# Kernel tuning notes

Hardware: AMD Instinct MI355X
Metric: run time of the kernel (lower is better)

## Reference

```python
import jax, jax.numpy as jnp
import numpy as np

E = 256  # embed_dim (hardcoded in source module)
H = 4    # n_head
D = E // H
SEQ = 32768


def setup_inputs() -> dict:
    key = jax.random.key(0)
    ks = jax.random.split(key, 5)
    x = jax.random.normal(ks[0], (SEQ, E), dtype=jnp.float32)
    in_proj_weight = jax.random.normal(ks[1], (3 * E, E), dtype=jnp.float32) * (1.0 / np.sqrt(E))
    in_proj_bias = jax.random.normal(ks[2], (3 * E,), dtype=jnp.float32) * 0.02
    out_proj_weight = jax.random.normal(ks[3], (E, E), dtype=jnp.float32) * (1.0 / np.sqrt(E))
    out_proj_bias = jax.random.normal(ks[4], (E,), dtype=jnp.float32) * 0.02
    return {
        "x": x,
        "in_proj_weight": in_proj_weight,
        "in_proj_bias": in_proj_bias,
        "out_proj_weight": out_proj_weight,
        "out_proj_bias": out_proj_bias,
    }


def reference(x, in_proj_weight, in_proj_bias, out_proj_weight, out_proj_bias):
    # QKV projections (q uses only the first token of x: single-query decode attention)
    Wq, Wk, Wv = in_proj_weight[:E], in_proj_weight[E:2 * E], in_proj_weight[2 * E:]
    bq, bk, bv = in_proj_bias[:E], in_proj_bias[E:2 * E], in_proj_bias[2 * E:]
    q = x[:1] @ Wq.T + bq            # [1, E]
    k = x @ Wk.T + bk                # [S, E]
    v = x @ Wv.T + bv                # [S, E]

    qh = q.reshape(H, D)             # [H, D] (single query)
    kh = k.reshape(-1, H, D)         # [S, H, D]
    vh = v.reshape(-1, H, D)         # [S, H, D]

    scale = 1.0 / np.sqrt(D).astype(np.float32)
    scores = jnp.einsum("hd,shd->hs", qh, kh) * scale   # [H, S]
    attn = jax.nn.softmax(scores, axis=-1)                # [H, S]
    ctx = jnp.einsum("hs,shd->hd", attn, vh)             # [H, D]

    out = ctx.reshape(1, E) @ out_proj_weight.T + out_proj_bias  # [1, E]
    return out
```

## Files before the change

kernel.cpp:

```cpp
#include <hip/hip_runtime.h>
#include <hip/hip_cooperative_groups.h>
namespace cg = cooperative_groups;

#define NBLK 256
#define WS_LP   0
#define WS_YV   1024
#define WS_B2   2048
#define WS_KQ   2304
#define WS_C4   3328
#define WS_M2   3392
#define WS_YP   265536

__device__ __forceinline__ float dot4(float4 a, float4 b) {
  return a.x * b.x + a.y * b.y + a.z * b.z + a.w * b.w;
}

__device__ __forceinline__ void phaseA_dist(const float* __restrict__ x, const float* __restrict__ W,
                                            const float* __restrict__ inb, float* __restrict__ kq,
                                            float* __restrict__ c4, float* qls, int bid, int t) {
  const int lane = t & 63, w = t >> 6;
  const int h = bid >> 6;
  const int c0 = (bid & 63) * 4;
  const int rloc = lane >> 3, sub = lane & 7;
  const int row = h * 64 + w * 8 + rloc;
  const float4* w4 = (const float4*)&W[(size_t)row * 256 + sub * 32];
  const float4* x4 = (const float4*)&x[sub * 32];
  float p = 0.f;
#pragma unroll
  for (int j = 0; j < 8; ++j) p += dot4(w4[j], x4[j]);
  p += __shfl_xor(p, 1);
  p += __shfl_xor(p, 2);
  p += __shfl_xor(p, 4);
  if (sub == 0) qls[w * 8 + rloc] = p + inb[row];
  __syncthreads();
  if (w < 4) {
    float v = W[(size_t)(256 + h * 64 + lane) * 256 + (c0 + w)] * qls[lane];
#pragma unroll
    for (int m = 1; m < 64; m <<= 1) v += __shfl_xor(v, m);
    if (lane == 0) kq[h * 256 + c0 + w] = v;
  } else if (w == 4 && (bid & 63) == 0) {
    float v = inb[256 + h * 64 + lane] * qls[lane];
#pragma unroll
    for (int m = 1; m < 64; m <<= 1) v += __shfl_xor(v, m);
    if (lane == 0) c4[h] = v;
  }
}

__device__ __forceinline__ void phaseA_m2(const float* __restrict__ W, const float* __restrict__ Wout,
                                          float* __restrict__ M2, float* sh, int b2, int t) {
  float* wout_t = sh;
  const int tile = b2 >> 1, sub = b2 & 1;
  const int h = tile >> 4, e0 = (tile & 15) * 16 + sub * 8;
  {
    const int e = t >> 6, d = t & 63;
    wout_t[e * 64 + d] = Wout[(size_t)(e0 + e) * 256 + h * 64 + d];
  }
  __syncthreads();
  const int c = t & 255, eh = t >> 8;
  float acc[4] = {0.f, 0.f, 0.f, 0.f};
#pragma unroll 8
  for (int d = 0; d < 64; ++d) {
    const float wv = W[(size_t)(512 + h * 64 + d) * 256 + c];
#pragma unroll
    for (int e = 0; e < 4; ++e) acc[e] += wv * wout_t[(eh * 4 + e) * 64 + d];
  }
#pragma unroll
  for (int e = 0; e < 4; ++e)
    M2[(size_t)(e0 + eh * 4 + e) * 1024 + h * 256 + c] = acc[e];
}

__device__ __forceinline__ void phaseA_b2(const float* __restrict__ Wout, const float* __restrict__ inb,
                                          const float* __restrict__ bout, float* __restrict__ bias2,
                                          float* sh, int b, int t) {
  float* red = sh;
  const int og = t >> 5, seg = t & 31;
  const int e = b * 16 + og;
  float acc = 0.f;
#pragma unroll
  for (int j = 0; j < 8; ++j)
    acc += Wout[(size_t)e * 256 + seg * 8 + j] * inb[512 + seg * 8 + j];
  red[og * 32 + seg] = acc;
  __syncthreads();
  if (t < 16) {
    float s = bout[b * 16 + t];
#pragma unroll
    for (int i = 0; i < 32; ++i) s += red[t * 32 + i];
    bias2[b * 16 + t] = s;
  }
}

__device__ __forceinline__ float bscore(float4 xv, float4 kq0, float4 kq1, float4 kq2,
                                        float4 kq3, float c4v, int lane) {
  float p0 = dot4(xv, kq0), p1 = dot4(xv, kq1), p2 = dot4(xv, kq2), p3 = dot4(xv, kq3);
  const bool b1 = (lane & 2) != 0;
  float keep0 = b1 ? p2 : p0, send0 = b1 ? p0 : p2;
  keep0 += __shfl_xor(send0, 2);
  float keep1 = b1 ? p3 : p1, send1 = b1 ? p1 : p3;
  keep1 += __shfl_xor(send1, 2);
  const bool b0 = (lane & 1) != 0;
  float vv = b0 ? keep1 : keep0, sv = b0 ? keep0 : keep1;
  vv += __shfl_xor(sv, 1);
  vv += __shfl_xor(vv, 4);
  vv += __shfl_xor(vv, 8);
  vv += __shfl_xor(vv, 16);
  vv += __shfl_xor(vv, 32);
  return (vv + c4v) * 0.125f;
}

__device__ __forceinline__ void phaseB_core(const float4* xvA, const float4* xvB,
                                            const float* __restrict__ kq, const float* __restrict__ c4,
                                            float* __restrict__ ypart, float* __restrict__ lpart,
                                            float* yls, int bid, int t) {
  float* sll = yls + 8192;
  const int lane = t & 63, w = t >> 6;
  const int hme = lane & 3;
  const float4 kq0 = *(const float4*)&kq[0 * 256 + lane * 4];
  const float4 kq1 = *(const float4*)&kq[1 * 256 + lane * 4];
  const float4 kq2 = *(const float4*)&kq[2 * 256 + lane * 4];
  const float4 kq3 = *(const float4*)&kq[3 * 256 + lane * 4];
  const float c4v = c4[hme];

  float vA[8], vB[8];
#pragma unroll
  for (int r = 0; r < 8; ++r) vA[r] = bscore(xvA[r], kq0, kq1, kq2, kq3, c4v, lane);
#pragma unroll
  for (int r = 0; r < 8; ++r) vB[r] = bscore(xvB[r], kq0, kq1, kq2, kq3, c4v, lane);

  float l = 0.f;
  float4 a[4];
#pragma unroll
  for (int k = 0; k < 4; ++k) a[k] = (float4){0.f, 0.f, 0.f, 0.f};
#pragma unroll
  for (int r = 0; r < 8; ++r) {
    const float e0 = __expf(vA[r]);
    l += e0;
    const float e1 = __shfl_xor(e0, 1);
    const float e2 = __shfl_xor(e0, 2);
    const float e3 = __shfl_xor(e0, 3);
    a[0].x += e0 * xvA[r].x; a[0].y += e0 * xvA[r].y; a[0].z += e0 * xvA[r].z; a[0].w += e0 * xvA[r].w;
    a[1].x += e1 * xvA[r].x; a[1].y += e1 * xvA[r].y; a[1].z += e1 * xvA[r].z; a[1].w += e1 * xvA[r].w;
    a[2].x += e2 * xvA[r].x; a[2].y += e2 * xvA[r].y; a[2].z += e2 * xvA[r].z; a[2].w += e2 * xvA[r].w;
    a[3].x += e3 * xvA[r].x; a[3].y += e3 * xvA[r].y; a[3].z += e3 * xvA[r].z; a[3].w += e3 * xvA[r].w;
  }
#pragma unroll
  for (int r = 0; r < 8; ++r) {
    const float e0 = __expf(vB[r]);
    l += e0;
    const float e1 = __shfl_xor(e0, 1);
    const float e2 = __shfl_xor(e0, 2);
    const float e3 = __shfl_xor(e0, 3);
    a[0].x += e0 * xvB[r].x; a[0].y += e0 * xvB[r].y; a[0].z += e0 * xvB[r].z; a[0].w += e0 * xvB[r].w;
    a[1].x += e1 * xvB[r].x; a[1].y += e1 * xvB[r].y; a[1].z += e1 * xvB[r].z; a[1].w += e1 * xvB[r].w;
    a[2].x += e2 * xvB[r].x; a[2].y += e2 * xvB[r].y; a[2].z += e2 * xvB[r].z; a[2].w += e2 * xvB[r].w;
    a[3].x += e3 * xvB[r].x; a[3].y += e3 * xvB[r].y; a[3].z += e3 * xvB[r].z; a[3].w += e3 * xvB[r].w;
  }

  __syncthreads();
  if (lane < 4) sll[w * 4 + lane] = l;
#pragma unroll
  for (int k = 0; k < 4; ++k) {
    const int h = hme ^ k;
    *(float4*)&yls[w * 1024 + h * 256 + lane * 4] = a[k];
  }
  __syncthreads();

  if (t < 4) {
    float lb = 0.f;
#pragma unroll
    for (int i = 0; i < 8; ++i) lb += sll[i * 4 + t];
    lpart[t * NBLK + bid] = lb;
  }
  float* yp = &ypart[(size_t)bid * 1024];
#pragma unroll
  for (int o = t; o < 1024; o += 512) {
    float s = 0.f;
#pragma unroll
    for (int i = 0; i < 8; ++i) s += yls[i * 1024 + o];
    yp[o] = s;
  }
}

__device__ __forceinline__ void phaseC(const float* __restrict__ ypart, const float* __restrict__ lpart,
                                       float* __restrict__ z, float* sh, int bid, int t) {
  float* lred = sh;
  float* sred = sh + 256;
  const int h = bid >> 4;
  const int o0 = bid * 16;
  if (t < 256) lred[t] = lpart[h * 256 + t];
  __syncthreads();
  for (int s = 128; s > 0; s >>= 1) {
    if (t < s) lred[t] += lred[t + s];
    __syncthreads();
  }
  const float inv = 1.0f / lred[0];
  const int ol = t & 15, bg = t >> 4;
  float s = 0.f;
#pragma unroll
  for (int j = 0; j < 8; ++j) {
    const int b = bg * 8 + j;
    s += ypart[(size_t)b * 1024 + o0 + ol];
  }
  sred[bg * 16 + ol] = s;
  __syncthreads();
  if (t < 16) {
    float tot = 0.f;
#pragma unroll
    for (int g = 0; g < 32; ++g) tot += sred[g * 16 + t];
    z[o0 + t] = tot * inv;
  }
}

__device__ __forceinline__ void phaseD(const float* __restrict__ M2, const float* __restrict__ z,
                                       const float* __restrict__ bias2, float* __restrict__ out,
                                       float* sh, int bid, int t) {
  float* zls = sh;
  float* smo = sh + 1024;
  for (int i = t; i < 1024; i += 512) zls[i] = z[i];
  __syncthreads();
  const int og = t >> 5, seg = t & 31;
  const int e = bid * 16 + og;
  float acc = 0.f;
  const float4* m4 = (const float4*)&M2[(size_t)e * 1024 + seg * 32];
  const float4* z4 = (const float4*)&zls[seg * 32];
#pragma unroll
  for (int j = 0; j < 8; ++j) acc += dot4(m4[j], z4[j]);
  smo[og * 32 + seg] = acc;
  __syncthreads();
  if (t < 16) {
    float s = bias2[bid * 16 + t];
#pragma unroll
    for (int i = 0; i < 32; ++i) s += smo[t * 32 + i];
    out[bid * 16 + t] = s;
  }
}

__global__ void __launch_bounds__(512, 1) mha_coop(const float* __restrict__ x,
                                                   const float* __restrict__ W,
                                                   const float* __restrict__ inb,
                                                   const float* __restrict__ Wout,
                                                   const float* __restrict__ bout,
                                                   float* __restrict__ out,
                                                   float* __restrict__ ws) {
  __shared__ __align__(16) float sh[8224];
  const int t = threadIdx.x, bid = blockIdx.x;
  const int lane = t & 63, w = t >> 6;
  cg::grid_group grid = cg::this_grid();

  const int r0 = bid * 128 + w * 16;
  float4 xvA[8], xvB[8];
#pragma unroll
  for (int r = 0; r < 8; ++r)
    xvA[r] = *(const float4*)&x[(size_t)(r0 + r) * 256 + lane * 4];
#pragma unroll
  for (int r = 0; r < 8; ++r)
    xvB[r] = *(const float4*)&x[(size_t)(r0 + 8 + r) * 256 + lane * 4];

  phaseA_dist(x, W, inb, ws + WS_KQ, ws + WS_C4, sh, bid, t);

  grid.sync();
  phaseB_core(xvA, xvB, ws + WS_KQ, ws + WS_C4, ws + WS_YP, ws + WS_LP, sh, bid, t);
  grid.sync();
  if (bid < 64) phaseC(ws + WS_YP, ws + WS_LP, ws + WS_YV, sh, bid, t);
  else if (bid < 192) phaseA_m2(W, Wout, ws + WS_M2, sh, bid - 64, t);
  else if (bid < 208) phaseA_b2(Wout, inb, bout, ws + WS_B2, sh, bid - 192, t);
  grid.sync();
  if (bid < 16) phaseD(ws + WS_M2, ws + WS_YV, ws + WS_B2, out, sh, bid, t);
}

__global__ void __launch_bounds__(512) fb_A(const float* __restrict__ x, const float* __restrict__ W,
                                            const float* __restrict__ inb, float* __restrict__ ws) {
  __shared__ __align__(16) float sh[64];
  phaseA_dist(x, W, inb, ws + WS_KQ, ws + WS_C4, sh, blockIdx.x, threadIdx.x);
}
__global__ void __launch_bounds__(512) fb_B(const float* __restrict__ x, float* __restrict__ ws) {
  __shared__ __align__(16) float sh[8224];
  const int bid = blockIdx.x, t = threadIdx.x;
  const int lane = t & 63, w = t >> 6;
  const int r0 = bid * 128 + w * 16;
  float4 xvA[8], xvB[8];
#pragma unroll
  for (int r = 0; r < 8; ++r)
    xvA[r] = *(const float4*)&x[(size_t)(r0 + r) * 256 + lane * 4];
#pragma unroll
  for (int r = 0; r < 8; ++r)
    xvB[r] = *(const float4*)&x[(size_t)(r0 + 8 + r) * 256 + lane * 4];
  phaseB_core(xvA, xvB, ws + WS_KQ, ws + WS_C4, ws + WS_YP, ws + WS_LP, sh, bid, t);
}
__global__ void __launch_bounds__(512) fb_CM(const float* __restrict__ W, const float* __restrict__ Wout,
                                             const float* __restrict__ inb, const float* __restrict__ bout,
                                             float* __restrict__ ws) {
  __shared__ __align__(16) float sh[832];
  const int bid = blockIdx.x, t = threadIdx.x;
  if (bid < 64) phaseC(ws + WS_YP, ws + WS_LP, ws + WS_YV, sh, bid, t);
  else if (bid < 192) phaseA_m2(W, Wout, ws + WS_M2, sh, bid - 64, t);
  else if (bid < 208) phaseA_b2(Wout, inb, bout, ws + WS_B2, sh, bid - 192, t);
}
__global__ void __launch_bounds__(512) fb_D(float* __restrict__ out, float* __restrict__ ws) {
  __shared__ __align__(16) float sh[1536];
  phaseD(ws + WS_M2, ws + WS_YV, ws + WS_B2, out, sh, blockIdx.x, threadIdx.x);
}

extern "C" void kernel_launch(void* const* d_in, const int* in_sizes, int n_in,
                              void* d_out, int out_size, void* d_ws, size_t ws_size,
                              hipStream_t stream) {
  const float* x = (const float*)d_in[0];
  const float* W = (const float*)d_in[1];
  const float* inb = (const float*)d_in[2];
  const float* Wout = (const float*)d_in[3];
  const float* bout = (const float*)d_in[4];
  float* out = (float*)d_out;
  float* ws = (float*)d_ws;

  int dev = 0;
  (void)hipGetDevice(&dev);
  int coopAttr = 0, ncu = 0, occ = 0;
  bool coop = (hipDeviceGetAttribute(&coopAttr, hipDeviceAttributeCooperativeLaunch, dev) == hipSuccess) &&
              coopAttr != 0;
  coop = coop &&
         (hipDeviceGetAttribute(&ncu, hipDeviceAttributeMultiprocessorCount, dev) == hipSuccess);
  coop = coop &&
         (hipOccupancyMaxActiveBlocksPerMultiprocessor(&occ, mha_coop, 512, 0) == hipSuccess);
  coop = coop && (occ * ncu >= NBLK);

  if (coop) {
    void* args[] = {(void*)&x, (void*)&W, (void*)&inb, (void*)&Wout,
                    (void*)&bout, (void*)&out, (void*)&ws};
    if (hipLaunchCooperativeKernel((const void*)mha_coop, dim3(NBLK), dim3(512),
                                   args, 0, stream) == hipSuccess)
      return;
  }
  fb_A<<<NBLK, 512, 0, stream>>>(x, W, inb, ws);
  fb_B<<<NBLK, 512, 0, stream>>>(x, ws);
  fb_CM<<<208, 512, 0, stream>>>(W, Wout, inb, bout, ws);
  fb_D<<<16, 512, 0, stream>>>(out, ws);
}
```

Measured before the change: 31.79 us.

## Drop final grid sync via fixed-point atomic reduction and hoist M2/B2 precompute

Moves the weight-folding work (M2, bias2) into the first phase so it runs before the first grid sync instead of after the attention pass. Phase C and the output projection are fused: each of the 64 blocks computes its slice of z, multiplies it by its M2 columns, and accumulates into a fixed-point integer buffer with atomics. A ticket counter picks the last block to write the final output. This removes one grid-wide barrier and the separate phase D. The cost is fixed-point quantization error and extra atomic traffic.

```diff
diff --git a/kernel.cpp b/kernel.cpp
--- a/kernel.cpp
+++ b/kernel.cpp
@@ -3,13 +3,16 @@
 namespace cg = cooperative_groups;
 
 #define NBLK 256
+#define SCALE 4194304.0f
+#define INV_SCALE 2.38418579e-7f
 #define WS_LP   0
-#define WS_YV   1024
-#define WS_B2   2048
-#define WS_KQ   2304
-#define WS_C4   3328
-#define WS_M2   3392
-#define WS_YP   265536
+#define WS_B2   1024
+#define WS_KQ   1280
+#define WS_C4   2304
+#define WS_M2   2368
+#define WS_YP   264512
+#define WS_ACC  526656
+#define WS_TK   530752
 
 __device__ __forceinline__ float dot4(float4 a, float4 b) {
   return a.x * b.x + a.y * b.y + a.z * b.z + a.w * b.w;
@@ -180,10 +183,14 @@
   }
 }
 
-__device__ __forceinline__ void phaseC(const float* __restrict__ ypart, const float* __restrict__ lpart,
-                                       float* __restrict__ z, float* sh, int bid, int t) {
+__device__ __forceinline__ void phaseCF64(const float* __restrict__ ypart, const float* __restrict__ lpart,
+                                          const float* __restrict__ M2, const float* __restrict__ bias2,
+                                          float* __restrict__ out, int* __restrict__ out_acc,
+                                          int* __restrict__ ticket, float* sh, int bid, int t) {
   float* lred = sh;
   float* sred = sh + 256;
+  float* z = sh + 768;
+  __shared__ int tk;
   const int h = bid >> 4;
   const int o0 = bid * 16;
   if (t < 256) lred[t] = lpart[h * 256 + t];
@@ -196,41 +203,30 @@
   const int ol = t & 15, bg = t >> 4;
   float s = 0.f;
 #pragma unroll
-  for (int j = 0; j < 8; ++j) {
-    const int b = bg * 8 + j;
-    s += ypart[(size_t)b * 1024 + o0 + ol];
-  }
+  for (int j = 0; j < 8; ++j) s += ypart[(size_t)(bg * 8 + j) * 1024 + o0 + ol];
   sred[bg * 16 + ol] = s;
   __syncthreads();
   if (t < 16) {
     float tot = 0.f;
 #pragma unroll
     for (int g = 0; g < 32; ++g) tot += sred[g * 16 + t];
-    z[o0 + t] = tot * inv;
-  }
-}
-
-__device__ __forceinline__ void phaseD(const float* __restrict__ M2, const float* __restrict__ z,
-                                       const float* __restrict__ bias2, float* __restrict__ out,
-                                       float* sh, int bid, int t) {
-  float* zls = sh;
-  float* smo = sh + 1024;
-  for (int i = t; i < 1024; i += 512) zls[i] = z[i];
-  __syncthreads();
-  const int og = t >> 5, seg = t & 31;
-  const int e = bid * 16 + og;
-  float acc = 0.f;
-  const float4* m4 = (const float4*)&M2[(size_t)e * 1024 + seg * 32];
-  const float4* z4 = (const float4*)&zls[seg * 32];
-#pragma unroll
-  for (int j = 0; j < 8; ++j) acc += dot4(m4[j], z4[j]);
-  smo[og * 32 + seg] = acc;
-  __syncthreads();
-  if (t < 16) {
-    float s = bias2[bid * 16 + t];
-#pragma unroll
-    for (int i = 0; i < 32; ++i) s += smo[t * 32 + i];
-    out[bid * 16 + t] = s;
+    z[t] = tot * inv;
+  }
+  __syncthreads();
+  const int e = t >> 1, half = t & 1;
+  const float4* m4 = (const float4*)&M2[(size_t)e * 1024 + o0 + half * 8];
+  const float4* z4 = (const float4*)&z[half * 8];
+  float acc = dot4(m4[0], z4[0]) + dot4(m4[1], z4[1]);
+  acc += __shfl_xor(acc, 1);
+  if (half == 0) atomicAdd(&out_acc[e * 16], __float2int_rn(acc * SCALE));
+  __threadfence();
+  __syncthreads();
+  if (t == 0)
+    tk = __hip_atomic_fetch_add(ticket, 1, __ATOMIC_ACQ_REL, __HIP_MEMORY_SCOPE_AGENT);
+  __syncthreads();
+  if (tk == 63 && t < 256) {
+    int v = __hip_atomic_load(&out_acc[t * 16], __ATOMIC_RELAXED, __HIP_MEMORY_SCOPE_AGENT);
+    out[t] = (float)v * INV_SCALE + bias2[t];
   }
 }
 
@@ -244,6 +240,8 @@
   __shared__ __align__(16) float sh[8224];
   const int t = threadIdx.x, bid = blockIdx.x;
   const int lane = t & 63, w = t >> 6;
+  int* out_acc = (int*)(ws + WS_ACC);
+  int* ticket = (int*)(ws + WS_TK);
   cg::grid_group grid = cg::this_grid();
 
   const int r0 = bid * 128 + w * 16;
@@ -256,21 +254,42 @@
     xvB[r] = *(const float4*)&x[(size_t)(r0 + 8 + r) * 256 + lane * 4];
 
   phaseA_dist(x, W, inb, ws + WS_KQ, ws + WS_C4, sh, bid, t);
+
+  if (bid >= 64 && bid < 192) {
+    __syncthreads();
+    phaseA_m2(W, Wout, ws + WS_M2, sh, bid - 64, t);
+  } else if (bid >= 192 && bid < 208) {
+    __syncthreads();
+    phaseA_b2(Wout, inb, bout, ws + WS_B2, sh, bid - 192, t);
+  } else if (bid == 208) {
+    for (int j = t; j < 4096; j += 512) out_acc[j] = 0;
+    if (t == 0) *ticket = 0;
+  }
 
   grid.sync();
   phaseB_core(xvA, xvB, ws + WS_KQ, ws + WS_C4, ws + WS_YP, ws + WS_LP, sh, bid, t);
   grid.sync();
-  if (bid < 64) phaseC(ws + WS_YP, ws + WS_LP, ws + WS_YV, sh, bid, t);
-  else if (bid < 192) phaseA_m2(W, Wout, ws + WS_M2, sh, bid - 64, t);
-  else if (bid < 208) phaseA_b2(Wout, inb, bout, ws + WS_B2, sh, bid - 192, t);
-  grid.sync();
-  if (bid < 16) phaseD(ws + WS_M2, ws + WS_YV, ws + WS_B2, out, sh, bid, t);
-}
-
-__global__ void __launch_bounds__(512) fb_A(const float* __restrict__ x, const float* __restrict__ W,
-                                            const float* __restrict__ inb, float* __restrict__ ws) {
-  __shared__ __align__(16) float sh[64];
-  phaseA_dist(x, W, inb, ws + WS_KQ, ws + WS_C4, sh, blockIdx.x, threadIdx.x);
+  if (bid < 64)
+    phaseCF64(ws + WS_YP, ws + WS_LP, ws + WS_M2, ws + WS_B2, out, out_acc, ticket, sh, bid, t);
+}
+
+__global__ void __launch_bounds__(512) fb_pre(const float* __restrict__ x, const float* __restrict__ W,
+                                              const float* __restrict__ inb, const float* __restrict__ Wout,
+                                              const float* __restrict__ bout, float* __restrict__ ws) {
+  __shared__ __align__(16) float sh[832];
+  const int bid = blockIdx.x, t = threadIdx.x;
+  phaseA_dist(x, W, inb, ws + WS_KQ, ws + WS_C4, sh, bid, t);
+  if (bid >= 64 && bid < 192) {
+    __syncthreads();
+    phaseA_m2(W, Wout, ws + WS_M2, sh, bid - 64, t);
+  } else if (bid >= 192 && bid < 208) {
+    __syncthreads();
+    phaseA_b2(Wout, inb, bout, ws + WS_B2, sh, bid - 192, t);
+  } else if (bid == 208) {
+    int* out_acc = (int*)(ws + WS_ACC);
+    for (int j = t; j < 4096; j += 512) out_acc[j] = 0;
+    if (t == 0) *(int*)(ws + WS_TK) = 0;
+  }
 }
 __global__ void __launch_bounds__(512) fb_B(const float* __restrict__ x, float* __restrict__ ws) {
   __shared__ __align__(16) float sh[8224];
@@ -286,18 +305,10 @@
     xvB[r] = *(const float4*)&x[(size_t)(r0 + 8 + r) * 256 + lane * 4];
   phaseB_core(xvA, xvB, ws + WS_KQ, ws + WS_C4, ws + WS_YP, ws + WS_LP, sh, bid, t);
 }
-__global__ void __launch_bounds__(512) fb_CM(const float* __restrict__ W, const float* __restrict__ Wout,
-                                             const float* __restrict__ inb, const float* __restrict__ bout,
-                                             float* __restrict__ ws) {
-  __shared__ __align__(16) float sh[832];
-  const int bid = blockIdx.x, t = threadIdx.x;
-  if (bid < 64) phaseC(ws + WS_YP, ws + WS_LP, ws + WS_YV, sh, bid, t);
-  else if (bid < 192) phaseA_m2(W, Wout, ws + WS_M2, sh, bid - 64, t);
-  else if (bid < 208) phaseA_b2(Wout, inb, bout, ws + WS_B2, sh, bid - 192, t);
-}
-__global__ void __launch_bounds__(512) fb_D(float* __restrict__ out, float* __restrict__ ws) {
-  __shared__ __align__(16) float sh[1536];
-  phaseD(ws + WS_M2, ws + WS_YV, ws + WS_B2, out, sh, blockIdx.x, threadIdx.x);
+__global__ void __launch_bounds__(512) fb_CF(float* __restrict__ out, float* __restrict__ ws) {
+  __shared__ __align__(16) float sh[800];
+  phaseCF64(ws + WS_YP, ws + WS_LP, ws + WS_M2, ws + WS_B2, out,
+            (int*)(ws + WS_ACC), (int*)(ws + WS_TK), sh, blockIdx.x, threadIdx.x);
 }
 
 extern "C" void kernel_launch(void* const* d_in, const int* in_sizes, int n_in,
@@ -329,8 +340,7 @@
                                    args, 0, stream) == hipSuccess)
       return;
   }
-  fb_A<<<NBLK, 512, 0, stream>>>(x, W, inb, ws);
+  fb_pre<<<NBLK, 512, 0, stream>>>(x, W, inb, Wout, bout, ws);
   fb_B<<<NBLK, 512, 0, stream>>>(x, ws);
-  fb_CM<<<208, 512, 0, stream>>>(W, Wout, inb, bout, ws);
-  fb_D<<<16, 512, 0, stream>>>(out, ws);
-}
+  fb_CF<<<64, 512, 0, stream>>>(out, ws);
+}
```

Result: slower. 38.59 us (+21.4%).
